# Kernel optimization log

Hardware: AMD Instinct MI355X
Metric: run time of the kernel (lower is better)

## Reference

```python
import jax, jax.numpy as jnp
import numpy as np

B, S, D = 1, 2048, 2048
H, KV, HD = 32, 8, 64          # heads, kv heads, head_dim
WINDOW = 1024                  # sliding window (left), causal
ROPE_THETA = 10000.0


def setup_inputs() -> dict:
    key = jax.random.key(0)
    ks = jax.random.split(key, 5)
    scale = 1.0 / np.sqrt(D)
    x = jax.random.normal(ks[0], (B, S, D), dtype=jnp.float32)
    wq = jax.random.normal(ks[1], (D, H * HD), dtype=jnp.float32) * scale
    wk = jax.random.normal(ks[2], (D, KV * HD), dtype=jnp.float32) * scale
    wv = jax.random.normal(ks[3], (D, KV * HD), dtype=jnp.float32) * scale
    wo = jax.random.normal(ks[4], (H * HD, D), dtype=jnp.float32) * scale
    # RoPE frequencies: freqs_cis = exp(i * t * theta^{-2j/hd}), stored as cos/sin
    inv_freq = 1.0 / (ROPE_THETA ** (np.arange(0, HD, 2, dtype=np.float32) / HD))  # [HD/2]
    t = np.arange(S, dtype=np.float32)
    ang = np.outer(t, inv_freq)  # [S, HD/2]
    freqs_cos = jnp.asarray(np.cos(ang), dtype=jnp.float32)
    freqs_sin = jnp.asarray(np.sin(ang), dtype=jnp.float32)
    return {"x": x, "wq": wq, "wk": wk, "wv": wv, "wo": wo,
            "freqs_cos": freqs_cos, "freqs_sin": freqs_sin}


def _apply_rope(t, cos, sin):
    # t: [B,S,h,HD]; pairs (t[...,2i], t[...,2i+1]) form complex numbers
    tr = t.reshape(*t.shape[:-1], HD // 2, 2)
    a, b = tr[..., 0], tr[..., 1]
    c = cos[None, :, None, :]  # [1,S,1,HD/2]
    s = sin[None, :, None, :]
    ra = a * c - b * s
    rb = a * s + b * c
    return jnp.stack([ra, rb], axis=-1).reshape(t.shape)


def reference(x, wq, wk, wv, wo, freqs_cos, freqs_sin):
    q = (x @ wq).reshape(B, S, H, HD)
    k = (x @ wk).reshape(B, S, KV, HD)
    v = (x @ wv).reshape(B, S, KV, HD)
    q = _apply_rope(q, freqs_cos, freqs_sin)
    k = _apply_rope(k, freqs_cos, freqs_sin)
    # GQA: repeat kv heads to match query heads
    k = jnp.repeat(k, H // KV, axis=2)  # [B,S,H,HD]
    v = jnp.repeat(v, H // KV, axis=2)
    scale = jnp.asarray(1.0 / np.sqrt(HD), dtype=x.dtype)
    scores = jnp.einsum('bqhd,bkhd->bhqk', q, k) * scale  # [B,H,S,S]
    i = jnp.arange(S)[:, None]
    j = jnp.arange(S)[None, :]
    allowed = (j <= i) & (j >= i - WINDOW)  # causal + sliding window
    scores = jnp.where(allowed[None, None], scores, jnp.asarray(-1e30, dtype=scores.dtype))
    attn = jax.nn.softmax(scores, axis=-1)
    out = jnp.einsum('bhqk,bkhd->bqhd', attn, v).reshape(B, S, H * HD)
    return out @ wo
```

## Files before the change

kernel.cpp:

```cpp
#include <hip/hip_runtime.h>
#include <stdint.h>

typedef __bf16 bf16_t;
typedef __bf16 bf16x8 __attribute__((ext_vector_type(8)));
typedef __bf16 bf16x4 __attribute__((ext_vector_type(4)));
typedef float floatx4 __attribute__((ext_vector_type(4)));

#define AS3(p) ((__attribute__((address_space(3))) void*)(p))
#define AS1(p) ((__attribute__((address_space(1))) void*)(void*)(p))

__device__ __forceinline__ void tr_dev(const float* __restrict__ src, int ncols,
                                       bf16_t* __restrict__ dst, int bx, int by, int t,
                                       bf16_t (*T)[68]) {
  const int nt = bx * 64, kt = by * 64;
  const int r0 = t >> 4;
  const int c0 = (t & 15) << 2;
#pragma unroll
  for (int p = 0; p < 4; ++p) {
    const int row = p * 16 + r0;
    floatx4 v = *(const floatx4*)&src[(size_t)(kt + row) * ncols + nt + c0];
    bf16x4 b;
#pragma unroll
    for (int i = 0; i < 4; ++i) b[i] = (bf16_t)v[i];
    *(bf16x4*)&T[row][c0] = b;
  }
  __syncthreads();
#pragma unroll
  for (int p = 0; p < 4; ++p) {
    const int n = p * 16 + r0;
    bf16x4 tmp;
#pragma unroll
    for (int i = 0; i < 4; ++i) tmp[i] = T[c0 + i][n];
    *(bf16x4*)&dst[(size_t)(nt + n) * 2048 + kt + c0] = tmp;
  }
}

__global__ __launch_bounds__(256) void prep_k(const float* __restrict__ x,
                                              const float* __restrict__ wq,
                                              const float* __restrict__ wk,
                                              const float* __restrict__ wv,
                                              const float* __restrict__ wo,
                                              bf16_t* __restrict__ xb,
                                              bf16_t* __restrict__ wt) {
  __shared__ __align__(16) bf16_t T[64][68];
  const int b = blockIdx.x, tid = threadIdx.x;
  if (b < 2048) {
    const int i = (b * 256 + tid) * 8;
    floatx4 a = *(const floatx4*)&x[i];
    floatx4 c = *(const floatx4*)&x[i + 4];
    bf16x8 o;
#pragma unroll
    for (int j = 0; j < 4; ++j) { o[j] = (bf16_t)a[j]; o[4 + j] = (bf16_t)c[j]; }
    *(bf16x8*)&xb[i] = o;
  } else if (b < 3072) {
    const int t = b - 2048;
    tr_dev(wq, 2048, wt, t & 31, t >> 5, tid, T);
  } else if (b < 3328) {
    const int t = b - 3072;
    tr_dev(wk, 512, wt + (size_t)2048 * 2048, t & 7, t >> 3, tid, T);
  } else if (b < 3584) {
    const int t = b - 3328;
    tr_dev(wv, 512, wt + (size_t)2560 * 2048, t & 7, t >> 3, tid, T);
  } else {
    const int t = b - 3584;
    tr_dev(wo, 2048, wt + (size_t)3072 * 2048, t & 31, t >> 5, tid, T);
  }
}

template <int EPI>
__global__ __launch_bounds__(128) void gemm_k(const bf16_t* __restrict__ A,
                                              const bf16_t* __restrict__ Bt,
                                              bf16_t* __restrict__ o0,
                                              bf16_t* __restrict__ o1,
                                              bf16_t* __restrict__ o2,
                                              float* __restrict__ fo,
                                              const float* __restrict__ fcos,
                                              const float* __restrict__ fsin) {
  constexpr int K = 2048;
  __shared__ __align__(16) bf16_t As[64 * 64];
  __shared__ __align__(16) bf16_t Bs[128 * 64];
  const int tid = threadIdx.x;
  const int lane = tid & 63;
  const int w = tid >> 6;
  const int quad = lane >> 4;
  const int l15 = lane & 15;
  const int m0 = blockIdx.y * 64;
  const int n0 = blockIdx.x * 128;
  const int sr = lane >> 3;
  const int sc = ((lane & 7) ^ (sr & 7)) << 3;
  const bf16_t* gA = A + (size_t)(m0 + w * 32 + sr) * K + sc;
  const bf16_t* gB = Bt + (size_t)(n0 + w * 64 + sr) * K + sc;
  bf16_t* lA = &As[(w * 32) * 64];
  bf16_t* lB = &Bs[(w * 64) * 64];
  floatx4 acc[4][4] = {};

  for (int k0 = 0; k0 < K; k0 += 64) {
#pragma unroll
    for (int j = 0; j < 4; ++j)
      __builtin_amdgcn_global_load_lds(AS1(gA + (size_t)j * 8 * K + k0),
                                       AS3(lA + j * 8 * 64), 16, 0, 0);
#pragma unroll
    for (int j = 0; j < 8; ++j)
      __builtin_amdgcn_global_load_lds(AS1(gB + (size_t)j * 8 * K + k0),
                                       AS3(lB + j * 8 * 64), 16, 0, 0);
    __syncthreads();
#pragma unroll
    for (int kk = 0; kk < 2; ++kk) {
      const int co = ((kk * 4 + quad) ^ (l15 & 7)) << 3;
      bf16x8 af[4], bfr[4];
#pragma unroll
      for (int i = 0; i < 4; ++i) {
        af[i] = *(const bf16x8*)&As[(i * 16 + l15) * 64 + co];
        bfr[i] = *(const bf16x8*)&Bs[(w * 64 + i * 16 + l15) * 64 + co];
      }
#pragma unroll
      for (int mi = 0; mi < 4; ++mi)
#pragma unroll
        for (int ni = 0; ni < 4; ++ni)
          acc[mi][ni] =
              __builtin_amdgcn_mfma_f32_16x16x32_bf16(af[mi], bfr[ni], acc[mi][ni], 0, 0, 0);
    }
    __syncthreads();
  }

  if constexpr (EPI == 0) {
#pragma unroll
    for (int ni = 0; ni < 4; ++ni) {
      const int col = n0 + w * 64 + ni * 16 + l15;
#pragma unroll
      for (int mi = 0; mi < 4; ++mi) {
        const int sb = m0 + mi * 16 + quad * 4;
        if (col < 2560) {
          const int fi = (col & 63) >> 1;
#pragma unroll
          for (int r = 0; r < 4; ++r) {
            const float v = acc[mi][ni][r];
            const float prt = __shfl_xor(v, 1);
            const int s = sb + r;
            const float c = fcos[s * 32 + fi];
            const float sn = fsin[s * 32 + fi];
            const float ov = (col & 1) ? (prt * sn + v * c) : (v * c - prt * sn);
            if (col < 2048)
              o0[(size_t)s * 2048 + col] = (bf16_t)ov;
            else
              o1[(size_t)s * 512 + (col - 2048)] = (bf16_t)ov;
          }
        } else {
          const int sp = (sb & ~31) | (quad * 8 + (mi & 1) * 4);
          bf16x4 pv;
#pragma unroll
          for (int r = 0; r < 4; ++r) pv[r] = (bf16_t)acc[mi][ni][r];
          *(bf16x4*)&o2[(size_t)(col - 2560) * 2048 + sp] = pv;
        }
      }
    }
  } else {
#pragma unroll
    for (int ni = 0; ni < 4; ++ni) {
      const int col = n0 + w * 64 + ni * 16 + l15;
#pragma unroll
      for (int mi = 0; mi < 4; ++mi) {
        const int sb = m0 + mi * 16 + quad * 4;
#pragma unroll
        for (int r = 0; r < 4; ++r) fo[(size_t)(sb + r) * 2048 + col] = acc[mi][ni][r];
      }
    }
  }
}

__global__ __launch_bounds__(256) void attn_k(const bf16_t* __restrict__ qb_,
                                              const bf16_t* __restrict__ kb_,
                                              const bf16_t* __restrict__ vt_,
                                              bf16_t* __restrict__ ob_) {
  __shared__ __align__(16) bf16_t sm[2][8 * 512];
  const int lane = threadIdx.x & 63, w = threadIdx.x >> 6;
  const int quad = lane >> 4, l15 = lane & 15;
  const int h = blockIdx.y, g = h >> 2;
  const int qb = (gridDim.x - 1 - blockIdx.x) * 64;
  const int qw = qb + w * 16;
  const int q = qw + l15;
  const bf16_t* qrow = qb_ + (size_t)q * 2048 + h * 64;
  const bf16x8 qf0 = *(const bf16x8*)(qrow + quad * 8);
  const bf16x8 qf1 = *(const bf16x8*)(qrow + 32 + quad * 8);
  floatx4 acc0 = {}, acc1 = {}, acc2 = {}, acc3 = {}, accl = {};
  const float SC = 0.125f * 1.44269504088896340736f;
  bf16x8 ones;
#pragma unroll
  for (int i = 0; i < 8; ++i) ones[i] = (bf16_t)1.0f;

  int kbB = qb - 1024;
  if (kbB < 0) kbB = 0;
  kbB &= ~31;
  const int nT = (qb + 64 - kbB) >> 5;
  int myS = qw - 1024;
  if (myS < 0) myS = 0;
  myS &= ~31;
  const int myE = qw + 16;

  const int lr = lane & 15, lc = lane >> 4;
  const bf16_t* gk = kb_ + (size_t)(kbB + (w >> 1) * 16 + lr) * 512 + g * 64 +
                     ((w & 1) * 4 + lc) * 8;
  const bf16_t* gv = vt_ + (size_t)(g * 64 + w * 16 + lr) * 2048 + kbB + lc * 8;

#define STAGE(bi, ti)                                                              \
  do {                                                                             \
    __builtin_amdgcn_global_load_lds(AS1(gk + (size_t)(ti) * (32 * 512)),          \
                                     AS3(&sm[bi][w * 512]), 16, 0, 0);             \
    __builtin_amdgcn_global_load_lds(AS1(gv + (size_t)(ti) * 32),                  \
                                     AS3(&sm[bi][(4 + w) * 512]), 16, 0, 0);       \
  } while (0)

#define MSK(pv, key)                                        \
  do {                                                      \
    if ((key) > q || (key) + 1024 < q) pv = -1.0e30f;       \
  } while (0)

  int kb = kbB;
  STAGE(0, 0);
  __syncthreads();
  for (int i = 0; i < nT; ++i, kb += 32) {
    if (i + 1 < nT) STAGE((i + 1) & 1, i + 1);
    if (kb >= myS && kb < myE) {
      const bf16_t* base = &sm[i & 1][(size_t)lane * 8];
      const bf16x8 k0 = *(const bf16x8*)(base);
      const bf16x8 k1 = *(const bf16x8*)(base + 512);
      const bf16x8 k2 = *(const bf16x8*)(base + 1024);
      const bf16x8 k3 = *(const bf16x8*)(base + 1536);
      const bf16x8 v0 = *(const bf16x8*)(base + 2048);
      const bf16x8 v1 = *(const bf16x8*)(base + 2560);
      const bf16x8 v2 = *(const bf16x8*)(base + 3072);
      const bf16x8 v3 = *(const bf16x8*)(base + 3584);
      floatx4 z0 = {}, z1 = {};
      z0 = __builtin_amdgcn_mfma_f32_16x16x32_bf16(k0, qf0, z0, 0, 0, 0);
      z0 = __builtin_amdgcn_mfma_f32_16x16x32_bf16(k1, qf1, z0, 0, 0, 0);
      z1 = __builtin_amdgcn_mfma_f32_16x16x32_bf16(k2, qf0, z1, 0, 0, 0);
      z1 = __builtin_amdgcn_mfma_f32_16x16x32_bf16(k3, qf1, z1, 0, 0, 0);
      float p0 = z0[0] * SC - 32.0f, p1 = z0[1] * SC - 32.0f;
      float p2 = z0[2] * SC - 32.0f, p3 = z0[3] * SC - 32.0f;
      float p4 = z1[0] * SC - 32.0f, p5 = z1[1] * SC - 32.0f;
      float p6 = z1[2] * SC - 32.0f, p7 = z1[3] * SC - 32.0f;
      if ((kb + 31 > qw) || (kb < qw - 1009)) {
        const int kq = kb + quad * 4;
        MSK(p0, kq + 0); MSK(p1, kq + 1); MSK(p2, kq + 2); MSK(p3, kq + 3);
        MSK(p4, kq + 16); MSK(p5, kq + 17); MSK(p6, kq + 18); MSK(p7, kq + 19);
      }
      bf16x8 pf;
      pf[0] = (bf16_t)__builtin_amdgcn_exp2f(p0);
      pf[1] = (bf16_t)__builtin_amdgcn_exp2f(p1);
      pf[2] = (bf16_t)__builtin_amdgcn_exp2f(p2);
      pf[3] = (bf16_t)__builtin_amdgcn_exp2f(p3);
      pf[4] = (bf16_t)__builtin_amdgcn_exp2f(p4);
      pf[5] = (bf16_t)__builtin_amdgcn_exp2f(p5);
      pf[6] = (bf16_t)__builtin_amdgcn_exp2f(p6);
      pf[7] = (bf16_t)__builtin_amdgcn_exp2f(p7);
      accl = __builtin_amdgcn_mfma_f32_16x16x32_bf16(ones, pf, accl, 0, 0, 0);
      acc0 = __builtin_amdgcn_mfma_f32_16x16x32_bf16(v0, pf, acc0, 0, 0, 0);
      acc1 = __builtin_amdgcn_mfma_f32_16x16x32_bf16(v1, pf, acc1, 0, 0, 0);
      acc2 = __builtin_amdgcn_mfma_f32_16x16x32_bf16(v2, pf, acc2, 0, 0, 0);
      acc3 = __builtin_amdgcn_mfma_f32_16x16x32_bf16(v3, pf, acc3, 0, 0, 0);
    }
    __syncthreads();
  }
#undef STAGE
#undef MSK

  const float inv = 1.0f / accl[0];
  bf16_t* obase = ob_ + (size_t)q * 2048 + h * 64 + quad * 4;
  bf16x4 ov;
#pragma unroll
  for (int r = 0; r < 4; ++r) ov[r] = (bf16_t)(acc0[r] * inv);
  *(bf16x4*)(obase) = ov;
#pragma unroll
  for (int r = 0; r < 4; ++r) ov[r] = (bf16_t)(acc1[r] * inv);
  *(bf16x4*)(obase + 16) = ov;
#pragma unroll
  for (int r = 0; r < 4; ++r) ov[r] = (bf16_t)(acc2[r] * inv);
  *(bf16x4*)(obase + 32) = ov;
#pragma unroll
  for (int r = 0; r < 4; ++r) ov[r] = (bf16_t)(acc3[r] * inv);
  *(bf16x4*)(obase + 48) = ov;
}

extern "C" void kernel_launch(void* const* d_in, const int* in_sizes, int n_in, void* d_out,
                              int out_size, void* d_ws, size_t ws_size, hipStream_t stream) {
  (void)in_sizes;
  (void)n_in;
  (void)out_size;
  (void)ws_size;
  const float* x = (const float*)d_in[0];
  const float* wq = (const float*)d_in[1];
  const float* wk = (const float*)d_in[2];
  const float* wv = (const float*)d_in[3];
  const float* wo = (const float*)d_in[4];
  const float* fcos = (const float*)d_in[5];
  const float* fsin = (const float*)d_in[6];
  float* out = (float*)d_out;

  bf16_t* xb = (bf16_t*)d_ws;
  bf16_t* wt = xb + (size_t)2048 * 2048;
  bf16_t* qbuf = wt + (size_t)5120 * 2048;
  bf16_t* kbuf = qbuf + (size_t)2048 * 2048;
  bf16_t* vtb = kbuf + (size_t)2048 * 512;
  bf16_t* att = vtb + (size_t)512 * 2048;

  prep_k<<<4608, 256, 0, stream>>>(x, wq, wk, wv, wo, xb, wt);
  gemm_k<0><<<dim3(24, 32), 128, 0, stream>>>(xb, wt, qbuf, kbuf, vtb, nullptr, fcos, fsin);
  attn_k<<<dim3(32, 32), 256, 0, stream>>>(qbuf, kbuf, vtb, att);
  gemm_k<1><<<dim3(16, 32), 128, 0, stream>>>(att, wt + (size_t)3072 * 2048, nullptr, nullptr,
                                              nullptr, out, fcos, fsin);
}
```

Measured before the change: 233.2 us.

## Split K across wave pairs in GEMM with LDS reduction of accumulators

Doubles GEMM block size to four waves, with each wave pair computing the same 64x64 output tile over different halves of each 64-wide K chunk. Partial accumulators are then summed through shared memory in two staged exchanges, and each wave writes half the tile in the epilogue. The aim is better latency hiding and MFMA utilisation from more waves per block. The cost is extra LDS traffic, additional barriers and fewer MFMAs per barrier.

After: 233.0 us. No clear change (-0.1%).

```diff
diff --git a/kernel.cpp b/kernel.cpp
--- a/kernel.cpp
+++ b/kernel.cpp
@@ -68,7 +68,7 @@
 }
 
 template <int EPI>
-__global__ __launch_bounds__(128) void gemm_k(const bf16_t* __restrict__ A,
+__global__ __launch_bounds__(256) void gemm_k(const bf16_t* __restrict__ A,
                                               const bf16_t* __restrict__ Bt,
                                               bf16_t* __restrict__ o0,
                                               bf16_t* __restrict__ o1,
@@ -88,84 +88,105 @@
   const int n0 = blockIdx.x * 128;
   const int sr = lane >> 3;
   const int sc = ((lane & 7) ^ (sr & 7)) << 3;
-  const bf16_t* gA = A + (size_t)(m0 + w * 32 + sr) * K + sc;
-  const bf16_t* gB = Bt + (size_t)(n0 + w * 64 + sr) * K + sc;
-  bf16_t* lA = &As[(w * 32) * 64];
-  bf16_t* lB = &Bs[(w * 64) * 64];
+  const bf16_t* gA = A + (size_t)(m0 + w * 16 + sr) * K + sc;
+  const bf16_t* gB = Bt + (size_t)(n0 + w * 32 + sr) * K + sc;
+  bf16_t* lA = &As[w * 1024];
+  bf16_t* lB = &Bs[w * 2048];
+  const int co = (((w & 1) * 4 + quad) ^ (l15 & 7)) << 3;
+  const int nbase = (w >> 1) * 64;
   floatx4 acc[4][4] = {};
 
   for (int k0 = 0; k0 < K; k0 += 64) {
+    __builtin_amdgcn_global_load_lds(AS1(gA + k0), AS3(lA), 16, 0, 0);
+    __builtin_amdgcn_global_load_lds(AS1(gA + 8 * K + k0), AS3(lA + 512), 16, 0, 0);
 #pragma unroll
     for (int j = 0; j < 4; ++j)
-      __builtin_amdgcn_global_load_lds(AS1(gA + (size_t)j * 8 * K + k0),
-                                       AS3(lA + j * 8 * 64), 16, 0, 0);
-#pragma unroll
-    for (int j = 0; j < 8; ++j)
       __builtin_amdgcn_global_load_lds(AS1(gB + (size_t)j * 8 * K + k0),
-                                       AS3(lB + j * 8 * 64), 16, 0, 0);
-    __syncthreads();
-#pragma unroll
-    for (int kk = 0; kk < 2; ++kk) {
-      const int co = ((kk * 4 + quad) ^ (l15 & 7)) << 3;
-      bf16x8 af[4], bfr[4];
-#pragma unroll
-      for (int i = 0; i < 4; ++i) {
-        af[i] = *(const bf16x8*)&As[(i * 16 + l15) * 64 + co];
-        bfr[i] = *(const bf16x8*)&Bs[(w * 64 + i * 16 + l15) * 64 + co];
-      }
-#pragma unroll
-      for (int mi = 0; mi < 4; ++mi)
-#pragma unroll
-        for (int ni = 0; ni < 4; ++ni)
-          acc[mi][ni] =
-              __builtin_amdgcn_mfma_f32_16x16x32_bf16(af[mi], bfr[ni], acc[mi][ni], 0, 0, 0);
+                                       AS3(lB + j * 512), 16, 0, 0);
+    __syncthreads();
+    bf16x8 af[4], bfr[4];
+#pragma unroll
+    for (int i = 0; i < 4; ++i) {
+      af[i] = *(const bf16x8*)&As[(i * 16 + l15) * 64 + co];
+      bfr[i] = *(const bf16x8*)&Bs[(nbase + i * 16 + l15) * 64 + co];
     }
-    __syncthreads();
-  }
-
+#pragma unroll
+    for (int mi = 0; mi < 4; ++mi)
+#pragma unroll
+      for (int ni = 0; ni < 4; ++ni)
+        acc[mi][ni] =
+            __builtin_amdgcn_mfma_f32_16x16x32_bf16(af[mi], bfr[ni], acc[mi][ni], 0, 0, 0);
+    __syncthreads();
+  }
+
+  {
+    float* xch = (float*)Bs;
+    float* wp = xch + w * 1024 + lane * 4;
+    const float* rp = xch + (w ^ 1) * 1024 + lane * 4;
+#define XW(mi)                                                   \
+  {                                                              \
+    _Pragma("unroll") for (int ni = 0; ni < 4; ++ni)             \
+        *(floatx4*)(wp + ni * 256) = acc[mi][ni];                \
+  }
+#define XR(mi)                                                   \
+  {                                                              \
+    _Pragma("unroll") for (int ni = 0; ni < 4; ++ni) {           \
+      floatx4 t = *(const floatx4*)(rp + ni * 256);              \
+      acc[mi][ni] += t;                                          \
+    }                                                            \
+  }
+    if (w & 1) { XW(0); } else { XW(2); }
+    __syncthreads();
+    if (w & 1) { XR(2); } else { XR(0); }
+    __syncthreads();
+    if (w & 1) { XW(1); } else { XW(3); }
+    __syncthreads();
+    if (w & 1) { XR(3); } else { XR(1); }
+#undef XW
+#undef XR
+  }
+
+#define EPIA(mi)                                                                     \
+  {                                                                                  \
+    _Pragma("unroll") for (int ni = 0; ni < 4; ++ni) {                               \
+      const int col = n0 + nbase + ni * 16 + l15;                                    \
+      const int sb = m0 + (mi)*16 + quad * 4;                                        \
+      if (col < 2560) {                                                              \
+        const int fi = (col & 63) >> 1;                                              \
+        _Pragma("unroll") for (int r = 0; r < 4; ++r) {                              \
+          const float v = acc[mi][ni][r];                                            \
+          const float prt = __shfl_xor(v, 1);                                        \
+          const int s = sb + r;                                                      \
+          const float c = fcos[s * 32 + fi];                                         \
+          const float sn = fsin[s * 32 + fi];                                        \
+          const float ov = (col & 1) ? (prt * sn + v * c) : (v * c - prt * sn);      \
+          if (col < 2048) o0[(size_t)s * 2048 + col] = (bf16_t)ov;                   \
+          else o1[(size_t)s * 512 + (col - 2048)] = (bf16_t)ov;                      \
+        }                                                                            \
+      } else {                                                                       \
+        const int sp = (sb & ~31) | (quad * 8 + ((mi)&1) * 4);                       \
+        bf16x4 pv;                                                                   \
+        _Pragma("unroll") for (int r = 0; r < 4; ++r) pv[r] = (bf16_t)acc[mi][ni][r];\
+        *(bf16x4*)&o2[(size_t)(col - 2560) * 2048 + sp] = pv;                        \
+      }                                                                              \
+    }                                                                                \
+  }
+#define EPIB(mi)                                                                     \
+  {                                                                                  \
+    _Pragma("unroll") for (int ni = 0; ni < 4; ++ni) {                               \
+      const int col = n0 + nbase + ni * 16 + l15;                                    \
+      const int sb = m0 + (mi)*16 + quad * 4;                                        \
+      _Pragma("unroll") for (int r = 0; r < 4; ++r)                                  \
+          fo[(size_t)(sb + r) * 2048 + col] = acc[mi][ni][r];                        \
+    }                                                                                \
+  }
   if constexpr (EPI == 0) {
-#pragma unroll
-    for (int ni = 0; ni < 4; ++ni) {
-      const int col = n0 + w * 64 + ni * 16 + l15;
-#pragma unroll
-      for (int mi = 0; mi < 4; ++mi) {
-        const int sb = m0 + mi * 16 + quad * 4;
-        if (col < 2560) {
-          const int fi = (col & 63) >> 1;
-#pragma unroll
-          for (int r = 0; r < 4; ++r) {
-            const float v = acc[mi][ni][r];
-            const float prt = __shfl_xor(v, 1);
-            const int s = sb + r;
-            const float c = fcos[s * 32 + fi];
-            const float sn = fsin[s * 32 + fi];
-            const float ov = (col & 1) ? (prt * sn + v * c) : (v * c - prt * sn);
-            if (col < 2048)
-              o0[(size_t)s * 2048 + col] = (bf16_t)ov;
-            else
-              o1[(size_t)s * 512 + (col - 2048)] = (bf16_t)ov;
-          }
-        } else {
-          const int sp = (sb & ~31) | (quad * 8 + (mi & 1) * 4);
-          bf16x4 pv;
-#pragma unroll
-          for (int r = 0; r < 4; ++r) pv[r] = (bf16_t)acc[mi][ni][r];
-          *(bf16x4*)&o2[(size_t)(col - 2560) * 2048 + sp] = pv;
-        }
-      }
-    }
+    if (w & 1) { EPIA(2); EPIA(3); } else { EPIA(0); EPIA(1); }
   } else {
-#pragma unroll
-    for (int ni = 0; ni < 4; ++ni) {
-      const int col = n0 + w * 64 + ni * 16 + l15;
-#pragma unroll
-      for (int mi = 0; mi < 4; ++mi) {
-        const int sb = m0 + mi * 16 + quad * 4;
-#pragma unroll
-        for (int r = 0; r < 4; ++r) fo[(size_t)(sb + r) * 2048 + col] = acc[mi][ni][r];
-      }
-    }
-  }
+    if (w & 1) { EPIB(2); EPIB(3); } else { EPIB(0); EPIB(1); }
+  }
+#undef EPIA
+#undef EPIB
 }
 
 __global__ __launch_bounds__(256) void attn_k(const bf16_t* __restrict__ qb_,
@@ -304,8 +325,8 @@
   bf16_t* att = vtb + (size_t)512 * 2048;
 
   prep_k<<<4608, 256, 0, stream>>>(x, wq, wk, wv, wo, xb, wt);
-  gemm_k<0><<<dim3(24, 32), 128, 0, stream>>>(xb, wt, qbuf, kbuf, vtb, nullptr, fcos, fsin);
+  gemm_k<0><<<dim3(24, 32), 256, 0, stream>>>(xb, wt, qbuf, kbuf, vtb, nullptr, fcos, fsin);
   attn_k<<<dim3(32, 32), 256, 0, stream>>>(qbuf, kbuf, vtb, att);
-  gemm_k<1><<<dim3(16, 32), 128, 0, stream>>>(att, wt + (size_t)3072 * 2048, nullptr, nullptr,
+  gemm_k<1><<<dim3(16, 32), 256, 0, stream>>>(att, wt + (size_t)3072 * 2048, nullptr, nullptr,
                                               nullptr, out, fcos, fsin);
 }
```

## Double-buffer GEMM LDS with four waves and triple-buffer attention K/V loads

Applied to the files above, without the earlier changes.

The GEMM kernel moves from two to four waves per block. Each wave now owns a 64x32 output tile, and LDS is double-buffered so the next K-slice is loaded while the current one feeds the MFMAs, with one barrier per iteration instead of two. The attention kernel moves from two to three LDS buffers, prefetches two tiles ahead, and uses an explicit vmcnt wait plus s_barrier in place of the trailing __syncthreads. The aim is to hide global-to-LDS latency behind compute, at the cost of more LDS per block and more fragile hand-written synchronization.

Result: faster. 227.4 us (-2.5%).

```diff
diff --git a/kernel.cpp b/kernel.cpp
--- a/kernel.cpp
+++ b/kernel.cpp
@@ -68,7 +68,7 @@
 }
 
 template <int EPI>
-__global__ __launch_bounds__(128) void gemm_k(const bf16_t* __restrict__ A,
+__global__ __launch_bounds__(256) void gemm_k(const bf16_t* __restrict__ A,
                                               const bf16_t* __restrict__ Bt,
                                               bf16_t* __restrict__ o0,
                                               bf16_t* __restrict__ o1,
@@ -77,8 +77,8 @@
                                               const float* __restrict__ fcos,
                                               const float* __restrict__ fsin) {
   constexpr int K = 2048;
-  __shared__ __align__(16) bf16_t As[64 * 64];
-  __shared__ __align__(16) bf16_t Bs[128 * 64];
+  __shared__ __align__(16) bf16_t As[2][64 * 64];
+  __shared__ __align__(16) bf16_t Bs[2][128 * 64];
   const int tid = threadIdx.x;
   const int lane = tid & 63;
   const int w = tid >> 6;
@@ -88,45 +88,52 @@
   const int n0 = blockIdx.x * 128;
   const int sr = lane >> 3;
   const int sc = ((lane & 7) ^ (sr & 7)) << 3;
-  const bf16_t* gA = A + (size_t)(m0 + w * 32 + sr) * K + sc;
-  const bf16_t* gB = Bt + (size_t)(n0 + w * 64 + sr) * K + sc;
-  bf16_t* lA = &As[(w * 32) * 64];
-  bf16_t* lB = &Bs[(w * 64) * 64];
-  floatx4 acc[4][4] = {};
-
-  for (int k0 = 0; k0 < K; k0 += 64) {
-#pragma unroll
-    for (int j = 0; j < 4; ++j)
-      __builtin_amdgcn_global_load_lds(AS1(gA + (size_t)j * 8 * K + k0),
-                                       AS3(lA + j * 8 * 64), 16, 0, 0);
-#pragma unroll
-    for (int j = 0; j < 8; ++j)
-      __builtin_amdgcn_global_load_lds(AS1(gB + (size_t)j * 8 * K + k0),
-                                       AS3(lB + j * 8 * 64), 16, 0, 0);
+  const bf16_t* gA = A + (size_t)(m0 + w * 16 + sr) * K + sc;
+  const bf16_t* gB = Bt + (size_t)(n0 + w * 32 + sr) * K + sc;
+  floatx4 acc[4][2] = {};
+
+#define GSTAGE(bi, k0v)                                                            \
+  do {                                                                             \
+    __builtin_amdgcn_global_load_lds(AS1(gA + (k0v)), AS3(&As[bi][w * 1024]), 16,  \
+                                     0, 0);                                        \
+    __builtin_amdgcn_global_load_lds(AS1(gA + 8 * K + (k0v)),                      \
+                                     AS3(&As[bi][w * 1024 + 512]), 16, 0, 0);      \
+    _Pragma("unroll") for (int j = 0; j < 4; ++j)                                  \
+        __builtin_amdgcn_global_load_lds(AS1(gB + (size_t)j * 8 * K + (k0v)),      \
+                                         AS3(&Bs[bi][w * 2048 + j * 512]), 16, 0,  \
+                                         0);                                       \
+  } while (0)
+
+  GSTAGE(0, 0);
+  for (int i = 0; i < 32; ++i) {
     __syncthreads();
+    if (i + 1 < 32) GSTAGE((i + 1) & 1, (i + 1) * 64);
+    const bf16_t* as = As[i & 1];
+    const bf16_t* bs = Bs[i & 1];
 #pragma unroll
     for (int kk = 0; kk < 2; ++kk) {
       const int co = ((kk * 4 + quad) ^ (l15 & 7)) << 3;
-      bf16x8 af[4], bfr[4];
-#pragma unroll
-      for (int i = 0; i < 4; ++i) {
-        af[i] = *(const bf16x8*)&As[(i * 16 + l15) * 64 + co];
-        bfr[i] = *(const bf16x8*)&Bs[(w * 64 + i * 16 + l15) * 64 + co];
-      }
+      bf16x8 af[4], bfr[2];
+#pragma unroll
+      for (int ii = 0; ii < 4; ++ii)
+        af[ii] = *(const bf16x8*)&as[(ii * 16 + l15) * 64 + co];
+#pragma unroll
+      for (int ii = 0; ii < 2; ++ii)
+        bfr[ii] = *(const bf16x8*)&bs[(w * 32 + ii * 16 + l15) * 64 + co];
 #pragma unroll
       for (int mi = 0; mi < 4; ++mi)
 #pragma unroll
-        for (int ni = 0; ni < 4; ++ni)
+        for (int ni = 0; ni < 2; ++ni)
           acc[mi][ni] =
               __builtin_amdgcn_mfma_f32_16x16x32_bf16(af[mi], bfr[ni], acc[mi][ni], 0, 0, 0);
     }
-    __syncthreads();
-  }
+  }
+#undef GSTAGE
 
   if constexpr (EPI == 0) {
 #pragma unroll
-    for (int ni = 0; ni < 4; ++ni) {
-      const int col = n0 + w * 64 + ni * 16 + l15;
+    for (int ni = 0; ni < 2; ++ni) {
+      const int col = n0 + w * 32 + ni * 16 + l15;
 #pragma unroll
       for (int mi = 0; mi < 4; ++mi) {
         const int sb = m0 + mi * 16 + quad * 4;
@@ -156,8 +163,8 @@
     }
   } else {
 #pragma unroll
-    for (int ni = 0; ni < 4; ++ni) {
-      const int col = n0 + w * 64 + ni * 16 + l15;
+    for (int ni = 0; ni < 2; ++ni) {
+      const int col = n0 + w * 32 + ni * 16 + l15;
 #pragma unroll
       for (int mi = 0; mi < 4; ++mi) {
         const int sb = m0 + mi * 16 + quad * 4;
@@ -172,7 +179,7 @@
                                               const bf16_t* __restrict__ kb_,
                                               const bf16_t* __restrict__ vt_,
                                               bf16_t* __restrict__ ob_) {
-  __shared__ __align__(16) bf16_t sm[2][8 * 512];
+  __shared__ __align__(16) bf16_t sm[3][8 * 512];
   const int lane = threadIdx.x & 63, w = threadIdx.x >> 6;
   const int quad = lane >> 4, l15 = lane & 15;
   const int h = blockIdx.y, g = h >> 2;
@@ -202,12 +209,12 @@
                      ((w & 1) * 4 + lc) * 8;
   const bf16_t* gv = vt_ + (size_t)(g * 64 + w * 16 + lr) * 2048 + kbB + lc * 8;
 
-#define STAGE(bi, ti)                                                              \
+#define STAGE(bi_, ti)                                                             \
   do {                                                                             \
     __builtin_amdgcn_global_load_lds(AS1(gk + (size_t)(ti) * (32 * 512)),          \
-                                     AS3(&sm[bi][w * 512]), 16, 0, 0);             \
+                                     AS3(&sm[bi_][w * 512]), 16, 0, 0);            \
     __builtin_amdgcn_global_load_lds(AS1(gv + (size_t)(ti) * 32),                  \
-                                     AS3(&sm[bi][(4 + w) * 512]), 16, 0, 0);       \
+                                     AS3(&sm[bi_][(4 + w) * 512]), 16, 0, 0);      \
   } while (0)
 
 #define MSK(pv, key)                                        \
@@ -217,11 +224,17 @@
 
   int kb = kbB;
   STAGE(0, 0);
-  __syncthreads();
+  STAGE(1, 1);
+  int bi = 0;
   for (int i = 0; i < nT; ++i, kb += 32) {
-    if (i + 1 < nT) STAGE((i + 1) & 1, i + 1);
+    asm volatile("s_waitcnt vmcnt(2)" ::: "memory");
+    __builtin_amdgcn_s_barrier();
+    asm volatile("" ::: "memory");
+    int p2 = bi - 1;
+    if (p2 < 0) p2 = 2;
+    if (i + 2 < nT) STAGE(p2, i + 2);
     if (kb >= myS && kb < myE) {
-      const bf16_t* base = &sm[i & 1][(size_t)lane * 8];
+      const bf16_t* base = &sm[bi][(size_t)lane * 8];
       const bf16x8 k0 = *(const bf16x8*)(base);
       const bf16x8 k1 = *(const bf16x8*)(base + 512);
       const bf16x8 k2 = *(const bf16x8*)(base + 1024);
@@ -236,18 +249,18 @@
       z1 = __builtin_amdgcn_mfma_f32_16x16x32_bf16(k2, qf0, z1, 0, 0, 0);
       z1 = __builtin_amdgcn_mfma_f32_16x16x32_bf16(k3, qf1, z1, 0, 0, 0);
       float p0 = z0[0] * SC - 32.0f, p1 = z0[1] * SC - 32.0f;
-      float p2 = z0[2] * SC - 32.0f, p3 = z0[3] * SC - 32.0f;
+      float p2f = z0[2] * SC - 32.0f, p3 = z0[3] * SC - 32.0f;
       float p4 = z1[0] * SC - 32.0f, p5 = z1[1] * SC - 32.0f;
       float p6 = z1[2] * SC - 32.0f, p7 = z1[3] * SC - 32.0f;
       if ((kb + 31 > qw) || (kb < qw - 1009)) {
         const int kq = kb + quad * 4;
-        MSK(p0, kq + 0); MSK(p1, kq + 1); MSK(p2, kq + 2); MSK(p3, kq + 3);
+        MSK(p0, kq + 0); MSK(p1, kq + 1); MSK(p2f, kq + 2); MSK(p3, kq + 3);
         MSK(p4, kq + 16); MSK(p5, kq + 17); MSK(p6, kq + 18); MSK(p7, kq + 19);
       }
       bf16x8 pf;
       pf[0] = (bf16_t)__builtin_amdgcn_exp2f(p0);
       pf[1] = (bf16_t)__builtin_amdgcn_exp2f(p1);
-      pf[2] = (bf16_t)__builtin_amdgcn_exp2f(p2);
+      pf[2] = (bf16_t)__builtin_amdgcn_exp2f(p2f);
       pf[3] = (bf16_t)__builtin_amdgcn_exp2f(p3);
       pf[4] = (bf16_t)__builtin_amdgcn_exp2f(p4);
       pf[5] = (bf16_t)__builtin_amdgcn_exp2f(p5);
@@ -259,8 +272,9 @@
       acc2 = __builtin_amdgcn_mfma_f32_16x16x32_bf16(v2, pf, acc2, 0, 0, 0);
       acc3 = __builtin_amdgcn_mfma_f32_16x16x32_bf16(v3, pf, acc3, 0, 0, 0);
     }
-    __syncthreads();
-  }
+    bi = (bi == 2) ? 0 : bi + 1;
+  }
+  asm volatile("s_waitcnt vmcnt(0)" ::: "memory");
 #undef STAGE
 #undef MSK
 
@@ -304,8 +318,8 @@
   bf16_t* att = vtb + (size_t)512 * 2048;
 
   prep_k<<<4608, 256, 0, stream>>>(x, wq, wk, wv, wo, xb, wt);
-  gemm_k<0><<<dim3(24, 32), 128, 0, stream>>>(xb, wt, qbuf, kbuf, vtb, nullptr, fcos, fsin);
+  gemm_k<0><<<dim3(24, 32), 256, 0, stream>>>(xb, wt, qbuf, kbuf, vtb, nullptr, fcos, fsin);
   attn_k<<<dim3(32, 32), 256, 0, stream>>>(qbuf, kbuf, vtb, att);
-  gemm_k<1><<<dim3(16, 32), 128, 0, stream>>>(att, wt + (size_t)3072 * 2048, nullptr, nullptr,
+  gemm_k<1><<<dim3(16, 32), 256, 0, stream>>>(att, wt + (size_t)3072 * 2048, nullptr, nullptr,
                                               nullptr, out, fcos, fsin);
 }
```
